# Kernel optimization log

Measured on AMD Instinct MI355X. Metric: run time of the kernel, lower is better.

## Reference

```python
import jax, jax.numpy as jnp
import numpy as np

B, N, E, H, L = 32, 128, 128, 8, 4      # graphs, nodes/graph, emb, heads, layers
ATOM, BOND, K, M = 64, 15, 32, 16384    # atom_dim, bond_dim, rbf_K, n_edges
CUTOFF = 5.0
DH = E // H


def _ln(x, g, b):
    mu = x.mean(-1, keepdims=True)
    var = ((x - mu) ** 2).mean(-1, keepdims=True)
    return (x - mu) / jnp.sqrt(var + 1e-5) * g + b


def setup_inputs() -> dict:
    key = jax.random.key(0)
    ks = iter(jax.random.split(key, 40))
    def rn(shape, s=1.0):
        return jax.random.normal(next(ks), shape, jnp.float32) * s
    inp = {}
    inp["x"] = rn((B * N, ATOM))
    inp["ei"] = jax.random.randint(next(ks), (2, M), 0, B * N, jnp.int32)
    bf = rn((M, BOND))
    dist = jax.random.uniform(next(ks), (M, 1), jnp.float32, 0.0, CUTOFF)
    inp["ea"] = jnp.concatenate([bf, dist], axis=1)  # last col = distance
    inp["pos"] = rn((B * N, 3), 2.0)
    inp["batch"] = jnp.repeat(jnp.arange(B, dtype=jnp.int32), N)  # contiguous equal-size graphs
    s = 0.02
    inp["Wproj"] = rn((ATOM, E), s); inp["bproj"] = jnp.zeros((E,), jnp.float32)
    EIN = BOND + K
    inp["Wlin"] = rn((EIN, E * E), s); inp["blin"] = jnp.zeros((E * E,), jnp.float32)
    inp["g_en"] = jnp.ones((E,), jnp.float32); inp["b_en"] = jnp.zeros((E,), jnp.float32)
    for nm in ["Wq", "Wk", "Wv", "Wo"]:
        inp[nm] = rn((L, E, E), s)
    for nm in ["bq", "bk", "bv", "bo"]:
        inp[nm] = jnp.zeros((L, E), jnp.float32)
    inp["g1"] = jnp.ones((L, E), jnp.float32); inp["b1"] = jnp.zeros((L, E), jnp.float32)
    inp["W1"] = rn((L, E, 2 * E), s); inp["bf1"] = jnp.zeros((L, 2 * E), jnp.float32)
    inp["W2"] = rn((L, 2 * E, E), s); inp["bf2"] = jnp.zeros((L, E), jnp.float32)
    inp["g2"] = jnp.ones((L, E), jnp.float32); inp["b2"] = jnp.zeros((L, E), jnp.float32)
    return inp


def reference(x, ei, ea, pos, batch, Wproj, bproj, Wlin, blin, g_en, b_en,
              Wq, bq, Wk, bk, Wv, bv, Wo, bo, g1, b1, W1, bf1, W2, bf2, g2, b2):
    # node projection
    h = x @ Wproj + bproj                              # [BN, E]
    # GaussianRBF on last edge-attr column
    d = jnp.clip(ea[:, -1], 0.0, 10.0)
    centers = jnp.linspace(0.0, CUTOFF, K)
    gamma = (CUTOFF / (K - 1)) ** -2
    rbf = jnp.exp(-gamma * (d[:, None] - centers) ** 2)  # [M, K]
    ea2 = jnp.concatenate([ea[:, :-1], rbf], axis=1)     # [M, BOND+K]
    # EdgeNetwork: gather -> per-edge matvec -> scatter-add -> LN
    m = (ea2 @ Wlin + blin).reshape(M, E, E)             # [M, E, E]
    msg = jnp.einsum('mef,mf->me', m, h[ei[1]])          # [M, E]
    agg = jnp.zeros_like(h).at[ei[0]].add(msg)
    h = _ln(h + agg, g_en, b_en)
    # batch-to-dense (equal-size contiguous graphs -> reshape)
    xp = h.reshape(B, N, E)
    pb = pos.reshape(B, N, 3)
    d2 = jnp.sum((pb[:, :, None, :] - pb[:, None, :, :]) ** 2, axis=-1)  # [B, N, N]
    db = jnp.where(d2 > 0, jnp.sqrt(jnp.where(d2 > 0, d2, 1.0)), 0.0)    # cdist
    mask = jnp.ones((B, N), bool)
    inv_sqrt_dh = 1.0 / np.sqrt(DH)
    for l in range(L):
        q = (xp @ Wq[l] + bq[l]).reshape(B, N, H, DH)
        k = (xp @ Wk[l] + bk[l]).reshape(B, N, H, DH)
        v = (xp @ Wv[l] + bv[l]).reshape(B, N, H, DH)
        sc = jnp.einsum('bihd,bjhd->bhij', q, k) * inv_sqrt_dh + db[:, None]
        sc = jnp.clip(sc, -10.0, 10.0)
        sc = jnp.where(mask[:, None, None, :], sc, -jnp.inf)
        a = jax.nn.softmax(sc, axis=-1)
        o = jnp.einsum('bhij,bjhd->bihd', a, v).reshape(B, N, E)
        att = o @ Wo[l] + bo[l]
        x1 = _ln(xp + att, g1[l], b1[l])
        ff = jax.nn.relu(x1 @ W1[l] + bf1[l]) @ W2[l] + bf2[l]
        xp = _ln(x1 + ff, g2[l], b2[l])
    mf = mask.astype(xp.dtype)[:, :, None]
    return (xp * mf).sum(1) / (mf.sum(1) + 1e-8)      # [B, E]
```

## Files before the change

kernel.cpp:

```cpp
#include <hip/hip_runtime.h>


typedef __attribute__((ext_vector_type(8))) short bf16x8;
typedef __attribute__((ext_vector_type(4))) float f32x4;
#define MFMA16(a, b, c) __builtin_amdgcn_mfma_f32_16x16x32_bf16(a, b, c, 0, 0, 0)

__device__ inline unsigned short f2bf(float f) {
  unsigned u = __float_as_uint(f);
  u = (u + 0x7FFF + ((u >> 16) & 1)) >> 16;
  return (unsigned short)u;
}
__device__ inline unsigned pack2(float a, float b) {
  return (unsigned)f2bf(a) | ((unsigned)f2bf(b) << 16);
}
__device__ inline float bf2f(unsigned short v) {
  return __uint_as_float(((unsigned)v) << 16);
}

__global__ __launch_bounds__(256) void k_setup(
    const float* __restrict__ x, const float* __restrict__ Wproj,
    const float* __restrict__ bproj, float* __restrict__ h,
    unsigned short* __restrict__ hb,
    const float* __restrict__ ea, float* __restrict__ ea2,
    const float* __restrict__ Wlin, const float* __restrict__ blin,
    unsigned short* __restrict__ wb,
    const float* __restrict__ Wq, const float* __restrict__ Wk,
    const float* __restrict__ Wv, const float* __restrict__ bq,
    const float* __restrict__ bk, const float* __restrict__ bv,
    unsigned short* __restrict__ qkvt, float* __restrict__ qkvb,
    const float* __restrict__ Wo, unsigned short* __restrict__ wot,
    const float* __restrict__ W1, unsigned short* __restrict__ w1t,
    const float* __restrict__ W2, unsigned short* __restrict__ w2t,
    float* __restrict__ agg) {
  __shared__ float xs[2][64];
  int blk = blockIdx.x, t = threadIdx.x;
  if (blk < 2048) {
    int sub = t >> 7, e = t & 127;
    int n = blk * 2 + sub;
    if (e < 64) xs[sub][e] = x[n * 64 + e];
    __syncthreads();
    float acc = bproj[e];
#pragma unroll
    for (int a = 0; a < 64; a++) acc += xs[sub][a] * Wproj[a * 128 + e];
    h[n * 128 + e] = acc;
    hb[n * 128 + e] = f2bf(acc);
    return;
  }
  int idx = (blk - 2048) * 256 + t;
  if (idx < 524288) {
    agg[idx] = 0.0f;
    return;
  }
  idx -= 524288;
  if (idx < 786432) {
    int m = idx / 48, c = idx % 48;
    float v;
    if (c < 15) {
      v = ea[m * 16 + c];
    } else if (c < 47) {
      int i = c - 15;
      float d = fminf(10.0f, fmaxf(0.0f, ea[m * 16 + 15]));
      float diff = d - 5.0f * (float)i / 31.0f;
      v = __expf(-38.44f * diff * diff);
    } else {
      v = 1.0f;
    }
    ea2[m * 48 + c] = v;
    return;
  }
  idx -= 786432;
  if (idx < 786432) {
    float v = (idx < 770048) ? Wlin[idx] : blin[idx - 770048];
    wb[idx] = f2bf(v);
    return;
  }
  idx -= 786432;
  if (idx < 196608) {
    int l = idx / 49152, r = idx % 49152;
    int j = r / 128, a = r % 128;
    int jj = j & 127;
    const float* W = (j < 128) ? Wq : (j < 256) ? Wk : Wv;
    qkvt[idx] = f2bf(W[l * 16384 + a * 128 + jj]);
    if (a == 0) {
      const float* bb = (j < 128) ? bq : (j < 256) ? bk : bv;
      qkvb[l * 384 + j] = bb[l * 128 + jj];
    }
    return;
  }
  idx -= 196608;
  if (idx < 65536) {
    int l = idx / 16384, r = idx % 16384;
    int a = r / 128, j = r % 128;
    wot[l * 16384 + j * 128 + a] = f2bf(Wo[idx]);
    return;
  }
  idx -= 65536;
  if (idx < 131072) {
    int l = idx / 32768, r = idx % 32768;
    int a = r / 256, j = r % 256;
    w1t[l * 32768 + j * 128 + a] = f2bf(W1[idx]);
    return;
  }
  idx -= 131072;
  {
    int l = idx / 32768, r = idx % 32768;
    int a = r / 128, j = r % 128;
    w2t[l * 32768 + j * 256 + a] = f2bf(W2[idx]);
  }
}

__global__ __launch_bounds__(256) void k_tbuild(const unsigned short* __restrict__ hb,
    const unsigned short* __restrict__ wb, unsigned short* __restrict__ T) {
  __shared__ unsigned short hs[16384];
  __shared__ unsigned short wsm[16384];
  int c = blockIdx.x >> 5;
  int n0 = (blockIdx.x & 31) << 7;
  int t = threadIdx.x;
  const uint4* hg = (const uint4*)hb + n0 * 16;
  const uint4* wg = (const uint4*)wb + c * 2048;
  uint4* hs4 = (uint4*)hs;
  uint4* ws4 = (uint4*)wsm;
#pragma unroll
  for (int i = 0; i < 8; i++) {
    int q = t + i * 256;
    int row = q >> 4, ch = q & 15;
    int d = row * 16 + (ch ^ (row & 7));
    hs4[d] = hg[q];
    ws4[d] = wg[q];
  }
  __syncthreads();
  int w = t >> 6, l = t & 63;
  int lr = l & 15, lg = l >> 4;
  f32x4 acc[2][8];
#pragma unroll
  for (int et = 0; et < 2; et++)
#pragma unroll
    for (int n = 0; n < 8; n++) acc[et][n] = (f32x4){0.f, 0.f, 0.f, 0.f};
#pragma unroll
  for (int s = 0; s < 4; s++) {
    bf16x8 af[2];
#pragma unroll
    for (int et = 0; et < 2; et++) {
      int er = w * 32 + et * 16 + lr;
      int ch = (s * 4 + lg) ^ (er & 7);
      af[et] = *(const bf16x8*)&wsm[(er * 16 + ch) * 8];
    }
#pragma unroll
    for (int n = 0; n < 8; n++) {
      int nr = n * 16 + lr;
      int ch = (s * 4 + lg) ^ (nr & 7);
      bf16x8 bfr = *(const bf16x8*)&hs[(nr * 16 + ch) * 8];
      acc[0][n] = MFMA16(af[0], bfr, acc[0][n]);
      acc[1][n] = MFMA16(af[1], bfr, acc[1][n]);
    }
  }
#pragma unroll
  for (int et = 0; et < 2; et++)
#pragma unroll
    for (int n = 0; n < 8; n++) {
      int node = n0 + n * 16 + lr;
      int e0 = w * 32 + et * 16 + lg * 4;
      uint2 pk;
      pk.x = pack2(acc[et][n][0], acc[et][n][1]);
      pk.y = pack2(acc[et][n][2], acc[et][n][3]);
      *(uint2*)&T[node * 6144 + c * 128 + e0] = pk;
    }
}

__global__ __launch_bounds__(128) void k_contract(const float* __restrict__ ea2,
    const int* __restrict__ ei, const unsigned short* __restrict__ T,
    float* __restrict__ agg) {
  int m = blockIdx.x, e = threadIdx.x;
  int src = ei[16384 + m], dst = ei[m];
  __shared__ float ec[48];
  if (e < 48) ec[e] = ea2[m * 48 + e];
  __syncthreads();
  const unsigned short* Ts = T + src * 6144;
  float acc = 0.0f;
#pragma unroll 6
  for (int c = 0; c < 48; c++) acc += ec[c] * bf2f(Ts[c * 128 + e]);
  atomicAdd(&agg[dst * 128 + e], acc);
}

__global__ __launch_bounds__(128) void k_ln(const float* __restrict__ in,
    const float* __restrict__ res, const float* __restrict__ g,
    const float* __restrict__ b, float* __restrict__ out) {
  int n = blockIdx.x, e = threadIdx.x;
  float v = in[n * 128 + e];
  if (res) v += res[n * 128 + e];
  float s = v, s2 = v * v;
#pragma unroll
  for (int o = 1; o < 64; o <<= 1) { s += __shfl_xor(s, o); s2 += __shfl_xor(s2, o); }
  __shared__ float r0[2], r1[2];
  int wid = e >> 6;
  if ((e & 63) == 0) { r0[wid] = s; r1[wid] = s2; }
  __syncthreads();
  float ts = r0[0] + r0[1], ts2 = r1[0] + r1[1];
  float mu = ts * (1.0f / 128.0f);
  float var = fmaxf(ts2 * (1.0f / 128.0f) - mu * mu, 0.0f);
  float inv = rsqrtf(var + 1e-5f);
  out[n * 128 + e] = (v - mu) * inv * g[e] + b[e];
}

__global__ __launch_bounds__(128) void k_dist(const float* __restrict__ pos, float* __restrict__ db) {
  int bi = blockIdx.x;
  int b = bi >> 7, i = bi & 127, j = threadIdx.x;
  float x0 = pos[(b * 128 + i) * 3 + 0];
  float y0 = pos[(b * 128 + i) * 3 + 1];
  float z0 = pos[(b * 128 + i) * 3 + 2];
  float dx = x0 - pos[(b * 128 + j) * 3 + 0];
  float dy = y0 - pos[(b * 128 + j) * 3 + 1];
  float dz = z0 - pos[(b * 128 + j) * 3 + 2];
  float d2 = dx * dx + dy * dy + dz * dz;
  db[b * 16384 + i * 128 + j] = (d2 > 0.0f) ? sqrtf(d2) : 0.0f;
}

template <int RELU, int RES, int LN, int KCH>
__global__ __launch_bounds__(256) void k_gemm(
    const float* __restrict__ A, const unsigned short* __restrict__ Bt,
    const float* __restrict__ bias, const float* __restrict__ res,
    const float* __restrict__ g, const float* __restrict__ bb,
    float* __restrict__ out, int ldc) {
  constexpr int K = KCH * 128;
  __shared__ unsigned short As[16384];
  __shared__ unsigned short Bs[16384];
  __shared__ float red[2][4][128];
  int t = threadIdx.x;
  int m0 = blockIdx.x << 7;
  int n0 = blockIdx.y << 7;
  uint4* As4 = (uint4*)As;
  uint4* Bs4 = (uint4*)Bs;
  int w = t >> 6, l = t & 63;
  int lr = l & 15, lg = l >> 4;

  f32x4 acc[2][8];
#pragma unroll
  for (int et = 0; et < 2; et++)
#pragma unroll
    for (int n = 0; n < 8; n++) acc[et][n] = (f32x4){0.f, 0.f, 0.f, 0.f};

  for (int kc = 0; kc < KCH; kc++) {
    if (kc) __syncthreads();
#pragma unroll
    for (int i = 0; i < 8; i++) {
      int q = t + i * 256;
      int row = q >> 4, ch = q & 15;
      int d = row * 16 + (ch ^ (row & 7));
      const float* ap = A + (size_t)(m0 + row) * K + kc * 128 + ch * 8;
      float4 fa = *(const float4*)ap;
      float4 fb = *(const float4*)(ap + 4);
      uint4 pk;
      pk.x = pack2(fa.x, fa.y); pk.y = pack2(fa.z, fa.w);
      pk.z = pack2(fb.x, fb.y); pk.w = pack2(fb.z, fb.w);
      As4[d] = pk;
      Bs4[d] = *((const uint4*)(Bt + (size_t)(n0 + row) * K + kc * 128) + ch);
    }
    __syncthreads();
#pragma unroll
    for (int s = 0; s < 4; s++) {
      bf16x8 af[2];
#pragma unroll
      for (int et = 0; et < 2; et++) {
        int er = w * 32 + et * 16 + lr;
        int ch = (s * 4 + lg) ^ (er & 7);
        af[et] = *(const bf16x8*)&Bs[(er * 16 + ch) * 8];
      }
#pragma unroll
      for (int n = 0; n < 8; n++) {
        int nr = n * 16 + lr;
        int ch = (s * 4 + lg) ^ (nr & 7);
        bf16x8 bfr = *(const bf16x8*)&As[(nr * 16 + ch) * 8];
        acc[0][n] = MFMA16(af[0], bfr, acc[0][n]);
        acc[1][n] = MFMA16(af[1], bfr, acc[1][n]);
      }
    }
  }

  float4 b4[2];
#pragma unroll
  for (int et = 0; et < 2; et++)
    b4[et] = *(const float4*)&bias[n0 + w * 32 + et * 16 + lg * 4];
  float v[2][8][4];
#pragma unroll
  for (int et = 0; et < 2; et++)
#pragma unroll
    for (int n = 0; n < 8; n++) {
      int node = m0 + n * 16 + lr;
      float4 rv;
      if (RES) rv = *(const float4*)&res[(size_t)node * 128 + w * 32 + et * 16 + lg * 4];
#pragma unroll
      for (int r = 0; r < 4; r++) {
        float xv = acc[et][n][r] + ((const float*)&b4[et])[r];
        if (RELU) xv = fmaxf(xv, 0.0f);
        if (RES) xv += ((const float*)&rv)[r];
        v[et][n][r] = xv;
      }
    }

  if (LN) {
    float s[8], s2[8];
#pragma unroll
    for (int n = 0; n < 8; n++) {
      float a = 0, b2s = 0;
#pragma unroll
      for (int et = 0; et < 2; et++)
#pragma unroll
        for (int r = 0; r < 4; r++) { a += v[et][n][r]; b2s += v[et][n][r] * v[et][n][r]; }
      s[n] = a; s2[n] = b2s;
    }
#pragma unroll
    for (int off = 16; off < 64; off <<= 1)
#pragma unroll
      for (int n = 0; n < 8; n++) { s[n] += __shfl_xor(s[n], off); s2[n] += __shfl_xor(s2[n], off); }
    if (l < 16) {
#pragma unroll
      for (int n = 0; n < 8; n++) { red[0][w][n * 16 + lr] = s[n]; red[1][w][n * 16 + lr] = s2[n]; }
    }
    __syncthreads();
    float4 g4[2], bb4[2];
#pragma unroll
    for (int et = 0; et < 2; et++) {
      g4[et]  = *(const float4*)&g[w * 32 + et * 16 + lg * 4];
      bb4[et] = *(const float4*)&bb[w * 32 + et * 16 + lg * 4];
    }
#pragma unroll
    for (int n = 0; n < 8; n++) {
      int nloc = n * 16 + lr;
      float ts  = red[0][0][nloc] + red[0][1][nloc] + red[0][2][nloc] + red[0][3][nloc];
      float ts2 = red[1][0][nloc] + red[1][1][nloc] + red[1][2][nloc] + red[1][3][nloc];
      float mu = ts * (1.0f / 128.0f);
      float var = fmaxf(ts2 * (1.0f / 128.0f) - mu * mu, 0.0f);
      float inv = rsqrtf(var + 1e-5f);
      int node = m0 + nloc;
#pragma unroll
      for (int et = 0; et < 2; et++) {
        float4 ov;
#pragma unroll
        for (int r = 0; r < 4; r++)
          ((float*)&ov)[r] = (v[et][n][r] - mu) * inv * ((const float*)&g4[et])[r] + ((const float*)&bb4[et])[r];
        *(float4*)&out[(size_t)node * ldc + w * 32 + et * 16 + lg * 4] = ov;
      }
    }
  } else {
#pragma unroll
    for (int et = 0; et < 2; et++)
#pragma unroll
      for (int n = 0; n < 8; n++) {
        int node = m0 + n * 16 + lr;
        float4 ov;
#pragma unroll
        for (int r = 0; r < 4; r++) ((float*)&ov)[r] = v[et][n][r];
        *(float4*)&out[(size_t)node * ldc + n0 + w * 32 + et * 16 + lg * 4] = ov;
      }
  }
}

__global__ __launch_bounds__(128) void k_attn(const float* __restrict__ qkv,
    const float* __restrict__ db, float* __restrict__ oatt) {
  __shared__ float ks[128][16], vs[128][16];
  int bh = blockIdx.x, b = bh >> 3, h = bh & 7;
  int i = threadIdx.x;
  int node = b * 128 + i;
  const float4* kr = (const float4*)(qkv + (size_t)node * 384 + 128 + h * 16);
  const float4* vr = (const float4*)(qkv + (size_t)node * 384 + 256 + h * 16);
#pragma unroll
  for (int d4 = 0; d4 < 4; d4++) {
    *(float4*)&ks[i][d4 * 4] = kr[d4];
    *(float4*)&vs[i][d4 * 4] = vr[d4];
  }
  float qr[16];
  const float4* qp = (const float4*)(qkv + (size_t)node * 384 + h * 16);
#pragma unroll
  for (int d4 = 0; d4 < 4; d4++) *(float4*)&qr[d4 * 4] = qp[d4];
  __syncthreads();
  const float4* dbr = (const float4*)(db + b * 16384 + i * 128);
  float rsum = 0.0f, o[16] = {};
  for (int j4 = 0; j4 < 32; j4++) {
    float4 dv = dbr[j4];
#pragma unroll
    for (int u = 0; u < 4; u++) {
      int j = j4 * 4 + u;
      float s = 0.0f;
#pragma unroll
      for (int d = 0; d < 16; d++) s += qr[d] * ks[j][d];
      s = s * 0.25f + ((const float*)&dv)[u];
      s = fminf(10.0f, fmaxf(-10.0f, s));
      float p = __expf(s);
      rsum += p;
#pragma unroll
      for (int d = 0; d < 16; d++) o[d] += p * vs[j][d];
    }
  }
  float r = 1.0f / rsum;
  float* op = oatt + (size_t)node * 128 + h * 16;
#pragma unroll
  for (int d4 = 0; d4 < 4; d4++)
    *(float4*)&op[d4 * 4] = make_float4(o[d4 * 4] * r, o[d4 * 4 + 1] * r, o[d4 * 4 + 2] * r, o[d4 * 4 + 3] * r);
}

__global__ __launch_bounds__(256) void k_layerout(
    const float* __restrict__ oatt, float* __restrict__ xp,
    const unsigned short* __restrict__ wot, const float* __restrict__ bo,
    const float* __restrict__ g1, const float* __restrict__ b1,
    const unsigned short* __restrict__ w1t, const float* __restrict__ bf1,
    const unsigned short* __restrict__ w2t, const float* __restrict__ bf2,
    const float* __restrict__ g2, const float* __restrict__ b2) {
  __shared__ unsigned short ffs[16384];
  __shared__ unsigned short x1s[8192];
  __shared__ unsigned short Bs[16384];
  __shared__ float red[2][4][64];
  int t = threadIdx.x;
  int m0 = blockIdx.x << 6;
  int w = t >> 6, l = t & 63, lr = l & 15, lg = l >> 4;

  {
    uint4* a4 = (uint4*)ffs;
#pragma unroll
    for (int i = 0; i < 4; i++) {
      int q = t + i * 256;
      int row = q >> 4, ch = q & 15;
      const float* ap = oatt + (size_t)(m0 + row) * 128 + ch * 8;
      float4 fa = *(const float4*)ap;
      float4 fb = *(const float4*)(ap + 4);
      uint4 pk;
      pk.x = pack2(fa.x, fa.y); pk.y = pack2(fa.z, fa.w);
      pk.z = pack2(fb.x, fb.y); pk.w = pack2(fb.z, fb.w);
      a4[row * 16 + (ch ^ (row & 7))] = pk;
    }
    uint4* b4p = (uint4*)Bs;
#pragma unroll
    for (int i = 0; i < 8; i++) {
      int q = t + i * 256;
      int row = q >> 4, ch = q & 15;
      b4p[row * 16 + (ch ^ (row & 7))] = *((const uint4*)(wot + (size_t)row * 128) + ch);
    }
  }
  __syncthreads();
  f32x4 acc[2][4];
#pragma unroll
  for (int et = 0; et < 2; et++)
#pragma unroll
    for (int n = 0; n < 4; n++) acc[et][n] = (f32x4){0.f, 0.f, 0.f, 0.f};
#pragma unroll
  for (int s = 0; s < 4; s++) {
    bf16x8 af[2];
#pragma unroll
    for (int et = 0; et < 2; et++) {
      int er = w * 32 + et * 16 + lr;
      int ch = (s * 4 + lg) ^ (er & 7);
      af[et] = *(const bf16x8*)&Bs[(er * 16 + ch) * 8];
    }
#pragma unroll
    for (int n = 0; n < 4; n++) {
      int nr = n * 16 + lr;
      int ch = (s * 4 + lg) ^ (nr & 7);
      bf16x8 bfr = *(const bf16x8*)&ffs[(nr * 16 + ch) * 8];
      acc[0][n] = MFMA16(af[0], bfr, acc[0][n]);
      acc[1][n] = MFMA16(af[1], bfr, acc[1][n]);
    }
  }
  float v1[2][4][4];
  {
    int e0 = w * 32 + lg * 4;
    float4 bo4[2] = { *(const float4*)&bo[e0], *(const float4*)&bo[e0 + 16] };
#pragma unroll
    for (int et = 0; et < 2; et++)
#pragma unroll
      for (int n = 0; n < 4; n++) {
        int node = m0 + n * 16 + lr;
        float4 rv = *(const float4*)&xp[(size_t)node * 128 + e0 + et * 16];
#pragma unroll
        for (int r = 0; r < 4; r++)
          v1[et][n][r] = acc[et][n][r] + ((const float*)&bo4[et])[r] + ((const float*)&rv)[r];
      }
    float s[4], s2[4];
#pragma unroll
    for (int n = 0; n < 4; n++) {
      float a = 0, b2s = 0;
#pragma unroll
      for (int et = 0; et < 2; et++)
#pragma unroll
        for (int r = 0; r < 4; r++) { a += v1[et][n][r]; b2s += v1[et][n][r] * v1[et][n][r]; }
      s[n] = a; s2[n] = b2s;
    }
#pragma unroll
    for (int off = 16; off < 64; off <<= 1)
#pragma unroll
      for (int n = 0; n < 4; n++) { s[n] += __shfl_xor(s[n], off); s2[n] += __shfl_xor(s2[n], off); }
    if (l < 16) {
#pragma unroll
      for (int n = 0; n < 4; n++) { red[0][w][n * 16 + lr] = s[n]; red[1][w][n * 16 + lr] = s2[n]; }
    }
    __syncthreads();
    float4 g4[2] = { *(const float4*)&g1[e0], *(const float4*)&g1[e0 + 16] };
    float4 bb4[2] = { *(const float4*)&b1[e0], *(const float4*)&b1[e0 + 16] };
#pragma unroll
    for (int n = 0; n < 4; n++) {
      int nloc = n * 16 + lr;
      float ts  = red[0][0][nloc] + red[0][1][nloc] + red[0][2][nloc] + red[0][3][nloc];
      float ts2 = red[1][0][nloc] + red[1][1][nloc] + red[1][2][nloc] + red[1][3][nloc];
      float mu = ts * (1.0f / 128.0f);
      float var = fmaxf(ts2 * (1.0f / 128.0f) - mu * mu, 0.0f);
      float inv = rsqrtf(var + 1e-5f);
#pragma unroll
      for (int et = 0; et < 2; et++) {
#pragma unroll
        for (int r = 0; r < 4; r++)
          v1[et][n][r] = (v1[et][n][r] - mu) * inv * ((const float*)&g4[et])[r] + ((const float*)&bb4[et])[r];
        int ch = w * 4 + et * 2 + (lg >> 1);
        uint2 pk;
        pk.x = pack2(v1[et][n][0], v1[et][n][1]);
        pk.y = pack2(v1[et][n][2], v1[et][n][3]);
        *(uint2*)&x1s[(nloc * 16 + (ch ^ (nloc & 7))) * 8 + (lg & 1) * 4] = pk;
      }
    }
  }
  __syncthreads();

  for (int ct = 0; ct < 2; ct++) {
    if (ct) __syncthreads();
    uint4* b4p = (uint4*)Bs;
#pragma unroll
    for (int i = 0; i < 8; i++) {
      int q = t + i * 256;
      int row = q >> 4, ch = q & 15;
      b4p[row * 16 + (ch ^ (row & 7))] =
          *((const uint4*)(w1t + (size_t)(ct * 128 + row) * 128) + ch);
    }
    __syncthreads();
#pragma unroll
    for (int et = 0; et < 2; et++)
#pragma unroll
      for (int n = 0; n < 4; n++) acc[et][n] = (f32x4){0.f, 0.f, 0.f, 0.f};
#pragma unroll
    for (int s = 0; s < 4; s++) {
      bf16x8 af[2];
#pragma unroll
      for (int et = 0; et < 2; et++) {
        int er = w * 32 + et * 16 + lr;
        int ch = (s * 4 + lg) ^ (er & 7);
        af[et] = *(const bf16x8*)&Bs[(er * 16 + ch) * 8];
      }
#pragma unroll
      for (int n = 0; n < 4; n++) {
        int nr = n * 16 + lr;
        int ch = (s * 4 + lg) ^ (nr & 7);
        bf16x8 bfr = *(const bf16x8*)&x1s[(nr * 16 + ch) * 8];
        acc[0][n] = MFMA16(af[0], bfr, acc[0][n]);
        acc[1][n] = MFMA16(af[1], bfr, acc[1][n]);
      }
    }
    int e0 = w * 32 + lg * 4;
    float4 bb0 = *(const float4*)&bf1[ct * 128 + e0];
    float4 bb1 = *(const float4*)&bf1[ct * 128 + e0 + 16];
#pragma unroll
    for (int et = 0; et < 2; et++) {
      const float* bbp = et ? (const float*)&bb1 : (const float*)&bb0;
#pragma unroll
      for (int n = 0; n < 4; n++) {
        int nloc = n * 16 + lr;
        float f0 = fmaxf(acc[et][n][0] + bbp[0], 0.0f);
        float f1 = fmaxf(acc[et][n][1] + bbp[1], 0.0f);
        float f2 = fmaxf(acc[et][n][2] + bbp[2], 0.0f);
        float f3 = fmaxf(acc[et][n][3] + bbp[3], 0.0f);
        int cg = ct * 16 + w * 4 + et * 2 + (lg >> 1);
        uint2 pk;
        pk.x = pack2(f0, f1);
        pk.y = pack2(f2, f3);
        *(uint2*)&ffs[(nloc * 32 + (cg ^ (nloc & 7))) * 8 + (lg & 1) * 4] = pk;
      }
    }
  }
  __syncthreads();

  f32x4 acc3[2][4];
#pragma unroll
  for (int et = 0; et < 2; et++)
#pragma unroll
    for (int n = 0; n < 4; n++) acc3[et][n] = (f32x4){0.f, 0.f, 0.f, 0.f};
  for (int kc = 0; kc < 2; kc++) {
    if (kc) __syncthreads();
    uint4* b4p = (uint4*)Bs;
#pragma unroll
    for (int i = 0; i < 8; i++) {
      int q = t + i * 256;
      int row = q >> 4, ch = q & 15;
      b4p[row * 16 + (ch ^ (row & 7))] =
          *((const uint4*)(w2t + (size_t)row * 256 + kc * 128) + ch);
    }
    __syncthreads();
#pragma unroll
    for (int s = 0; s < 4; s++) {
      bf16x8 af[2];
#pragma unroll
      for (int et = 0; et < 2; et++) {
        int er = w * 32 + et * 16 + lr;
        int ch = (s * 4 + lg) ^ (er & 7);
        af[et] = *(const bf16x8*)&Bs[(er * 16 + ch) * 8];
      }
#pragma unroll
      for (int n = 0; n < 4; n++) {
        int nr = n * 16 + lr;
        int gch = kc * 16 + s * 4 + lg;
        bf16x8 bfr = *(const bf16x8*)&ffs[(nr * 32 + (gch ^ (nr & 7))) * 8];
        acc3[0][n] = MFMA16(af[0], bfr, acc3[0][n]);
        acc3[1][n] = MFMA16(af[1], bfr, acc3[1][n]);
      }
    }
  }
  {
    int e0 = w * 32 + lg * 4;
    float4 bo4[2] = { *(const float4*)&bf2[e0], *(const float4*)&bf2[e0 + 16] };
    float v2[2][4][4];
#pragma unroll
    for (int et = 0; et < 2; et++)
#pragma unroll
      for (int n = 0; n < 4; n++)
#pragma unroll
        for (int r = 0; r < 4; r++)
          v2[et][n][r] = acc3[et][n][r] + ((const float*)&bo4[et])[r] + v1[et][n][r];
    float s[4], s2[4];
#pragma unroll
    for (int n = 0; n < 4; n++) {
      float a = 0, b2s = 0;
#pragma unroll
      for (int et = 0; et < 2; et++)
#pragma unroll
        for (int r = 0; r < 4; r++) { a += v2[et][n][r]; b2s += v2[et][n][r] * v2[et][n][r]; }
      s[n] = a; s2[n] = b2s;
    }
#pragma unroll
    for (int off = 16; off < 64; off <<= 1)
#pragma unroll
      for (int n = 0; n < 4; n++) { s[n] += __shfl_xor(s[n], off); s2[n] += __shfl_xor(s2[n], off); }
    __syncthreads();
    if (l < 16) {
#pragma unroll
      for (int n = 0; n < 4; n++) { red[0][w][n * 16 + lr] = s[n]; red[1][w][n * 16 + lr] = s2[n]; }
    }
    __syncthreads();
    float4 g4[2] = { *(const float4*)&g2[e0], *(const float4*)&g2[e0 + 16] };
    float4 bb4[2] = { *(const float4*)&b2[e0], *(const float4*)&b2[e0 + 16] };
#pragma unroll
    for (int n = 0; n < 4; n++) {
      int nloc = n * 16 + lr;
      float ts  = red[0][0][nloc] + red[0][1][nloc] + red[0][2][nloc] + red[0][3][nloc];
      float ts2 = red[1][0][nloc] + red[1][1][nloc] + red[1][2][nloc] + red[1][3][nloc];
      float mu = ts * (1.0f / 128.0f);
      float var = fmaxf(ts2 * (1.0f / 128.0f) - mu * mu, 0.0f);
      float inv = rsqrtf(var + 1e-5f);
      int node = m0 + nloc;
#pragma unroll
      for (int et = 0; et < 2; et++) {
        float4 ov;
#pragma unroll
        for (int r = 0; r < 4; r++)
          ((float*)&ov)[r] = (v2[et][n][r] - mu) * inv * ((const float*)&g4[et])[r] + ((const float*)&bb4[et])[r];
        *(float4*)&xp[(size_t)node * 128 + e0 + et * 16] = ov;
      }
    }
  }
}

__global__ __launch_bounds__(128) void k_pool(const float* __restrict__ xp, float* __restrict__ out) {
  int b = blockIdx.x, e = threadIdx.x;
  float s = 0.0f;
  for (int n = 0; n < 128; n++) s += xp[(b * 128 + n) * 128 + e];
  out[b * 128 + e] = s * (1.0f / 128.0f);
}

extern "C" void kernel_launch(void* const* d_in, const int* in_sizes, int n_in,
                              void* d_out, int out_size, void* d_ws, size_t ws_size,
                              hipStream_t stream) {
  const float* x     = (const float*)d_in[0];
  const int*   ei    = (const int*)  d_in[1];
  const float* ea    = (const float*)d_in[2];
  const float* pos   = (const float*)d_in[3];
  const float* Wproj = (const float*)d_in[5];
  const float* bproj = (const float*)d_in[6];
  const float* Wlin  = (const float*)d_in[7];
  const float* blin  = (const float*)d_in[8];
  const float* g_en  = (const float*)d_in[9];
  const float* b_en  = (const float*)d_in[10];
  const float* Wq    = (const float*)d_in[11];
  const float* Wk    = (const float*)d_in[12];
  const float* Wv    = (const float*)d_in[13];
  const float* Wo    = (const float*)d_in[14];
  const float* bq    = (const float*)d_in[15];
  const float* bk    = (const float*)d_in[16];
  const float* bv    = (const float*)d_in[17];
  const float* bo    = (const float*)d_in[18];
  const float* g1    = (const float*)d_in[19];
  const float* b1    = (const float*)d_in[20];
  const float* W1    = (const float*)d_in[21];
  const float* bf1   = (const float*)d_in[22];
  const float* W2    = (const float*)d_in[23];
  const float* bf2   = (const float*)d_in[24];
  const float* g2    = (const float*)d_in[25];
  const float* b2    = (const float*)d_in[26];

  float* ws = (float*)d_ws;
  float* ea2  = ws;
  float* hbuf = ea2  + 786432;
  float* agg  = hbuf + 524288;
  unsigned short* hbf  = (unsigned short*)(agg + 524288);
  unsigned short* wbf  = hbf + 524288;
  unsigned short* qkvt = wbf + 786432;
  unsigned short* wot  = qkvt + 196608;
  unsigned short* w1t  = wot + 65536;
  unsigned short* w2t  = w1t + 131072;
  float* qkvb = (float*)(w2t + 131072);
  float* base2 = qkvb + 1536;
  unsigned short* Tb = (unsigned short*)base2;
  float* db   = base2;
  float* xp   = db   + 524288;
  float* qkv  = xp   + 524288;
  float* oatt = qkv  + 1572864;

  k_setup<<<12288, 256, 0, stream>>>(x, Wproj, bproj, hbuf, hbf,
      ea, ea2, Wlin, blin, wbf, Wq, Wk, Wv, bq, bk, bv, qkvt, qkvb,
      Wo, wot, W1, w1t, W2, w2t, agg);
  k_tbuild<<<1536, 256, 0, stream>>>(hbf, wbf, Tb);
  k_contract<<<16384, 128, 0, stream>>>(ea2, ei, Tb, agg);
  k_ln<<<4096, 128, 0, stream>>>(agg, hbuf, g_en, b_en, xp);
  k_dist<<<4096, 128, 0, stream>>>(pos, db);

  for (int l = 0; l < 4; l++) {
    k_gemm<0, 0, 0, 1><<<dim3(32, 3), 256, 0, stream>>>(
        xp, qkvt + l * 49152, qkvb + l * 384, nullptr, nullptr, nullptr, qkv, 384);
    k_attn<<<256, 128, 0, stream>>>(qkv, db, oatt);
    k_layerout<<<64, 256, 0, stream>>>(oatt, xp,
        wot + l * 16384, bo + l * 128, g1 + l * 128, b1 + l * 128,
        w1t + l * 32768, bf1 + l * 256,
        w2t + l * 32768, bf2 + l * 128, g2 + l * 128, b2 + l * 128);
  }

  k_pool<<<32, 128, 0, stream>>>(xp, (float*)d_out);
}
```

Baseline: 336.8 us.

## Fuse edge message GEMM, LN+QKV, and next-layer QKV into layer-out kernel

Replaces the per-node T tensor build plus per-edge contraction with a single edge kernel. It gathers source-node features for 64 edges, runs an MFMA against each of the 48 weight slices, and accumulates the messages weighted by the edge attributes before doing atomic adds. The encoder LayerNorm is fused with the first QKV projection, each layer's output kernel also computes the next layer's QKV, and the distance matrix moves into the setup kernel. This removes the large T intermediate buffer and several launches. In exchange, each edge block reloads all 48 weight slices serially with a sync per slice, and only 256 blocks are launched.

```diff
diff --git a/kernel.cpp b/kernel.cpp
--- a/kernel.cpp
+++ b/kernel.cpp
@@ -12,9 +12,6 @@
 }
 __device__ inline unsigned pack2(float a, float b) {
   return (unsigned)f2bf(a) | ((unsigned)f2bf(b) << 16);
-}
-__device__ inline float bf2f(unsigned short v) {
-  return __uint_as_float(((unsigned)v) << 16);
 }
 
 __global__ __launch_bounds__(256) void k_setup(
@@ -31,7 +28,8 @@
     const float* __restrict__ Wo, unsigned short* __restrict__ wot,
     const float* __restrict__ W1, unsigned short* __restrict__ w1t,
     const float* __restrict__ W2, unsigned short* __restrict__ w2t,
-    float* __restrict__ agg) {
+    float* __restrict__ agg,
+    const float* __restrict__ pos, float* __restrict__ db) {
   __shared__ float xs[2][64];
   int blk = blockIdx.x, t = threadIdx.x;
   if (blk < 2048) {
@@ -47,10 +45,7 @@
     return;
   }
   int idx = (blk - 2048) * 256 + t;
-  if (idx < 524288) {
-    agg[idx] = 0.0f;
-    return;
-  }
+  if (idx < 524288) { agg[idx] = 0.0f; return; }
   idx -= 524288;
   if (idx < 786432) {
     int m = idx / 48, c = idx % 48;
@@ -102,171 +97,164 @@
     return;
   }
   idx -= 131072;
-  {
+  if (idx < 131072) {
     int l = idx / 32768, r = idx % 32768;
     int a = r / 128, j = r % 128;
     w2t[l * 32768 + j * 256 + a] = f2bf(W2[idx]);
-  }
-}
-
-__global__ __launch_bounds__(256) void k_tbuild(const unsigned short* __restrict__ hb,
-    const unsigned short* __restrict__ wb, unsigned short* __restrict__ T) {
-  __shared__ unsigned short hs[16384];
-  __shared__ unsigned short wsm[16384];
-  int c = blockIdx.x >> 5;
-  int n0 = (blockIdx.x & 31) << 7;
-  int t = threadIdx.x;
-  const uint4* hg = (const uint4*)hb + n0 * 16;
-  const uint4* wg = (const uint4*)wb + c * 2048;
+    return;
+  }
+  idx -= 131072;
+  {
+    int j = idx & 127, i2 = (idx >> 7) & 127, b = idx >> 14;
+    float x0 = pos[(b * 128 + i2) * 3 + 0];
+    float y0 = pos[(b * 128 + i2) * 3 + 1];
+    float z0 = pos[(b * 128 + i2) * 3 + 2];
+    float dx = x0 - pos[(b * 128 + j) * 3 + 0];
+    float dy = y0 - pos[(b * 128 + j) * 3 + 1];
+    float dz = z0 - pos[(b * 128 + j) * 3 + 2];
+    float d2 = dx * dx + dy * dy + dz * dz;
+    db[b * 16384 + i2 * 128 + j] = (d2 > 0.0f) ? sqrtf(d2) : 0.0f;
+  }
+}
+
+__global__ __launch_bounds__(256) void k_edge(const float* __restrict__ ea2,
+    const int* __restrict__ ei, const unsigned short* __restrict__ hbf,
+    const unsigned short* __restrict__ wb, float* __restrict__ agg) {
+  __shared__ unsigned short hs[8192];
+  __shared__ float et[64][48];
+  __shared__ unsigned short Bs[16384];
+  __shared__ int srcs[64], dsts[64];
+  int t = threadIdx.x, m0 = blockIdx.x * 64;
+  if (t < 64) { srcs[t] = ei[16384 + m0 + t]; dsts[t] = ei[m0 + t]; }
+  __syncthreads();
   uint4* hs4 = (uint4*)hs;
-  uint4* ws4 = (uint4*)wsm;
-#pragma unroll
-  for (int i = 0; i < 8; i++) {
+#pragma unroll
+  for (int i = 0; i < 4; i++) {
     int q = t + i * 256;
     int row = q >> 4, ch = q & 15;
-    int d = row * 16 + (ch ^ (row & 7));
-    hs4[d] = hg[q];
-    ws4[d] = wg[q];
-  }
-  __syncthreads();
-  int w = t >> 6, l = t & 63;
-  int lr = l & 15, lg = l >> 4;
-  f32x4 acc[2][8];
-#pragma unroll
-  for (int et = 0; et < 2; et++)
-#pragma unroll
-    for (int n = 0; n < 8; n++) acc[et][n] = (f32x4){0.f, 0.f, 0.f, 0.f};
-#pragma unroll
-  for (int s = 0; s < 4; s++) {
-    bf16x8 af[2];
-#pragma unroll
-    for (int et = 0; et < 2; et++) {
-      int er = w * 32 + et * 16 + lr;
-      int ch = (s * 4 + lg) ^ (er & 7);
-      af[et] = *(const bf16x8*)&wsm[(er * 16 + ch) * 8];
-    }
-#pragma unroll
-    for (int n = 0; n < 8; n++) {
-      int nr = n * 16 + lr;
-      int ch = (s * 4 + lg) ^ (nr & 7);
-      bf16x8 bfr = *(const bf16x8*)&hs[(nr * 16 + ch) * 8];
-      acc[0][n] = MFMA16(af[0], bfr, acc[0][n]);
-      acc[1][n] = MFMA16(af[1], bfr, acc[1][n]);
-    }
-  }
-#pragma unroll
-  for (int et = 0; et < 2; et++)
-#pragma unroll
-    for (int n = 0; n < 8; n++) {
-      int node = n0 + n * 16 + lr;
-      int e0 = w * 32 + et * 16 + lg * 4;
-      uint2 pk;
-      pk.x = pack2(acc[et][n][0], acc[et][n][1]);
-      pk.y = pack2(acc[et][n][2], acc[et][n][3]);
-      *(uint2*)&T[node * 6144 + c * 128 + e0] = pk;
-    }
-}
-
-__global__ __launch_bounds__(128) void k_contract(const float* __restrict__ ea2,
-    const int* __restrict__ ei, const unsigned short* __restrict__ T,
-    float* __restrict__ agg) {
-  int m = blockIdx.x, e = threadIdx.x;
-  int src = ei[16384 + m], dst = ei[m];
-  __shared__ float ec[48];
-  if (e < 48) ec[e] = ea2[m * 48 + e];
-  __syncthreads();
-  const unsigned short* Ts = T + src * 6144;
-  float acc = 0.0f;
-#pragma unroll 6
-  for (int c = 0; c < 48; c++) acc += ec[c] * bf2f(Ts[c * 128 + e]);
-  atomicAdd(&agg[dst * 128 + e], acc);
-}
-
-__global__ __launch_bounds__(128) void k_ln(const float* __restrict__ in,
-    const float* __restrict__ res, const float* __restrict__ g,
-    const float* __restrict__ b, float* __restrict__ out) {
-  int n = blockIdx.x, e = threadIdx.x;
-  float v = in[n * 128 + e];
-  if (res) v += res[n * 128 + e];
-  float s = v, s2 = v * v;
-#pragma unroll
-  for (int o = 1; o < 64; o <<= 1) { s += __shfl_xor(s, o); s2 += __shfl_xor(s2, o); }
-  __shared__ float r0[2], r1[2];
-  int wid = e >> 6;
-  if ((e & 63) == 0) { r0[wid] = s; r1[wid] = s2; }
-  __syncthreads();
-  float ts = r0[0] + r0[1], ts2 = r1[0] + r1[1];
-  float mu = ts * (1.0f / 128.0f);
-  float var = fmaxf(ts2 * (1.0f / 128.0f) - mu * mu, 0.0f);
-  float inv = rsqrtf(var + 1e-5f);
-  out[n * 128 + e] = (v - mu) * inv * g[e] + b[e];
-}
-
-__global__ __launch_bounds__(128) void k_dist(const float* __restrict__ pos, float* __restrict__ db) {
-  int bi = blockIdx.x;
-  int b = bi >> 7, i = bi & 127, j = threadIdx.x;
-  float x0 = pos[(b * 128 + i) * 3 + 0];
-  float y0 = pos[(b * 128 + i) * 3 + 1];
-  float z0 = pos[(b * 128 + i) * 3 + 2];
-  float dx = x0 - pos[(b * 128 + j) * 3 + 0];
-  float dy = y0 - pos[(b * 128 + j) * 3 + 1];
-  float dz = z0 - pos[(b * 128 + j) * 3 + 2];
-  float d2 = dx * dx + dy * dy + dz * dz;
-  db[b * 16384 + i * 128 + j] = (d2 > 0.0f) ? sqrtf(d2) : 0.0f;
-}
-
-template <int RELU, int RES, int LN, int KCH>
-__global__ __launch_bounds__(256) void k_gemm(
-    const float* __restrict__ A, const unsigned short* __restrict__ Bt,
-    const float* __restrict__ bias, const float* __restrict__ res,
-    const float* __restrict__ g, const float* __restrict__ bb,
-    float* __restrict__ out, int ldc) {
-  constexpr int K = KCH * 128;
-  __shared__ unsigned short As[16384];
-  __shared__ unsigned short Bs[16384];
-  __shared__ float red[2][4][128];
-  int t = threadIdx.x;
-  int m0 = blockIdx.x << 7;
-  int n0 = blockIdx.y << 7;
-  uint4* As4 = (uint4*)As;
+    hs4[row * 16 + (ch ^ (row & 7))] = ((const uint4*)(hbf + (size_t)srcs[row] * 128))[ch];
+  }
+#pragma unroll
+  for (int i = 0; i < 12; i++) {
+    int p = t + i * 256;
+    int mi = p / 48, c = p % 48;
+    et[mi][c] = ea2[(size_t)(m0 + mi) * 48 + c];
+  }
+  int w = t >> 6, l = t & 63, lr = l & 15, lg = l >> 4;
+  float msg[2][4][4] = {};
+  const f32x4 zf = {0.f, 0.f, 0.f, 0.f};
   uint4* Bs4 = (uint4*)Bs;
-  int w = t >> 6, l = t & 63;
-  int lr = l & 15, lg = l >> 4;
-
-  f32x4 acc[2][8];
-#pragma unroll
-  for (int et = 0; et < 2; et++)
-#pragma unroll
-    for (int n = 0; n < 8; n++) acc[et][n] = (f32x4){0.f, 0.f, 0.f, 0.f};
-
-  for (int kc = 0; kc < KCH; kc++) {
-    if (kc) __syncthreads();
+  for (int c = 0; c < 48; c++) {
+    __syncthreads();
 #pragma unroll
     for (int i = 0; i < 8; i++) {
       int q = t + i * 256;
       int row = q >> 4, ch = q & 15;
-      int d = row * 16 + (ch ^ (row & 7));
-      const float* ap = A + (size_t)(m0 + row) * K + kc * 128 + ch * 8;
-      float4 fa = *(const float4*)ap;
-      float4 fb = *(const float4*)(ap + 4);
-      uint4 pk;
-      pk.x = pack2(fa.x, fa.y); pk.y = pack2(fa.z, fa.w);
-      pk.z = pack2(fb.x, fb.y); pk.w = pack2(fb.z, fb.w);
-      As4[d] = pk;
-      Bs4[d] = *((const uint4*)(Bt + (size_t)(n0 + row) * K + kc * 128) + ch);
-    }
-    __syncthreads();
+      Bs4[row * 16 + (ch ^ (row & 7))] =
+          ((const uint4*)(wb + (size_t)c * 16384 + row * 128))[ch];
+    }
+    __syncthreads();
+    f32x4 pacc[2][4];
 #pragma unroll
     for (int s = 0; s < 4; s++) {
       bf16x8 af[2];
 #pragma unroll
-      for (int et = 0; et < 2; et++) {
-        int er = w * 32 + et * 16 + lr;
+      for (int e2 = 0; e2 < 2; e2++) {
+        int er = w * 32 + e2 * 16 + lr;
         int ch = (s * 4 + lg) ^ (er & 7);
-        af[et] = *(const bf16x8*)&Bs[(er * 16 + ch) * 8];
-      }
-#pragma unroll
-      for (int n = 0; n < 8; n++) {
+        af[e2] = *(const bf16x8*)&Bs[(er * 16 + ch) * 8];
+      }
+#pragma unroll
+      for (int n = 0; n < 4; n++) {
+        int nr = n * 16 + lr;
+        int ch = (s * 4 + lg) ^ (nr & 7);
+        bf16x8 bfr = *(const bf16x8*)&hs[(nr * 16 + ch) * 8];
+        if (s == 0) {
+          pacc[0][n] = MFMA16(af[0], bfr, zf);
+          pacc[1][n] = MFMA16(af[1], bfr, zf);
+        } else {
+          pacc[0][n] = MFMA16(af[0], bfr, pacc[0][n]);
+          pacc[1][n] = MFMA16(af[1], bfr, pacc[1][n]);
+        }
+      }
+    }
+#pragma unroll
+    for (int n = 0; n < 4; n++) {
+      float am = et[n * 16 + lr][c];
+#pragma unroll
+      for (int e2 = 0; e2 < 2; e2++)
+#pragma unroll
+        for (int r = 0; r < 4; r++)
+          msg[e2][n][r] += am * pacc[e2][n][r];
+    }
+  }
+#pragma unroll
+  for (int n = 0; n < 4; n++) {
+    int dst = dsts[n * 16 + lr];
+#pragma unroll
+    for (int e2 = 0; e2 < 2; e2++) {
+      int e0 = w * 32 + e2 * 16 + lg * 4;
+#pragma unroll
+      for (int r = 0; r < 4; r++)
+        atomicAdd(&agg[(size_t)dst * 128 + e0 + r], msg[e2][n][r]);
+    }
+  }
+}
+
+__global__ __launch_bounds__(256) void k_lnqkv(const float* __restrict__ agg,
+    const float* __restrict__ hbuf, const float* __restrict__ g_en,
+    const float* __restrict__ b_en, float* __restrict__ xp,
+    const unsigned short* __restrict__ qkvt, const float* __restrict__ qkvb,
+    float* __restrict__ qkv) {
+  __shared__ unsigned short As[8192];
+  __shared__ unsigned short Bs[16384];
+  int t = threadIdx.x, m0 = blockIdx.x * 64;
+  int w = t >> 6, l = t & 63, lr = l & 15, lg = l >> 4;
+  float ge0 = g_en[2 * l], ge1 = g_en[2 * l + 1];
+  float be0 = b_en[2 * l], be1 = b_en[2 * l + 1];
+  for (int i = 0; i < 16; i++) {
+    int r = i * 4 + w;
+    float2 av = ((const float2*)(agg + (size_t)(m0 + r) * 128))[l];
+    float2 hv = ((const float2*)(hbuf + (size_t)(m0 + r) * 128))[l];
+    float v0 = av.x + hv.x, v1 = av.y + hv.y;
+    float s = v0 + v1, s2 = v0 * v0 + v1 * v1;
+#pragma unroll
+    for (int o = 1; o < 64; o <<= 1) { s += __shfl_xor(s, o); s2 += __shfl_xor(s2, o); }
+    float mu = s * (1.0f / 128.0f);
+    float var = fmaxf(s2 * (1.0f / 128.0f) - mu * mu, 0.0f);
+    float inv = rsqrtf(var + 1e-5f);
+    float o0 = (v0 - mu) * inv * ge0 + be0;
+    float o1 = (v1 - mu) * inv * ge1 + be1;
+    ((float2*)(xp + (size_t)(m0 + r) * 128))[l] = make_float2(o0, o1);
+    ((unsigned*)As)[(r * 16 + ((l >> 2) ^ (r & 7))) * 4 + (l & 3)] = pack2(o0, o1);
+  }
+  uint4* Bs4 = (uint4*)Bs;
+  for (int cchunk = 0; cchunk < 3; cchunk++) {
+    __syncthreads();
+#pragma unroll
+    for (int i = 0; i < 8; i++) {
+      int q = t + i * 256;
+      int row = q >> 4, ch = q & 15;
+      Bs4[row * 16 + (ch ^ (row & 7))] =
+          ((const uint4*)(qkvt + (size_t)(cchunk * 128 + row) * 128))[ch];
+    }
+    __syncthreads();
+    f32x4 acc[2][4];
+#pragma unroll
+    for (int e2 = 0; e2 < 2; e2++)
+#pragma unroll
+      for (int n = 0; n < 4; n++) acc[e2][n] = (f32x4){0.f, 0.f, 0.f, 0.f};
+#pragma unroll
+    for (int s = 0; s < 4; s++) {
+      bf16x8 af[2];
+#pragma unroll
+      for (int e2 = 0; e2 < 2; e2++) {
+        int er = w * 32 + e2 * 16 + lr;
+        int ch = (s * 4 + lg) ^ (er & 7);
+        af[e2] = *(const bf16x8*)&Bs[(er * 16 + ch) * 8];
+      }
+#pragma unroll
+      for (int n = 0; n < 4; n++) {
         int nr = n * 16 + lr;
         int ch = (s * 4 + lg) ^ (nr & 7);
         bf16x8 bfr = *(const bf16x8*)&As[(nr * 16 + ch) * 8];
@@ -274,84 +262,19 @@
         acc[1][n] = MFMA16(af[1], bfr, acc[1][n]);
       }
     }
-  }
-
-  float4 b4[2];
-#pragma unroll
-  for (int et = 0; et < 2; et++)
-    b4[et] = *(const float4*)&bias[n0 + w * 32 + et * 16 + lg * 4];
-  float v[2][8][4];
-#pragma unroll
-  for (int et = 0; et < 2; et++)
-#pragma unroll
-    for (int n = 0; n < 8; n++) {
-      int node = m0 + n * 16 + lr;
-      float4 rv;
-      if (RES) rv = *(const float4*)&res[(size_t)node * 128 + w * 32 + et * 16 + lg * 4];
-#pragma unroll
-      for (int r = 0; r < 4; r++) {
-        float xv = acc[et][n][r] + ((const float*)&b4[et])[r];
-        if (RELU) xv = fmaxf(xv, 0.0f);
-        if (RES) xv += ((const float*)&rv)[r];
-        v[et][n][r] = xv;
-      }
-    }
-
-  if (LN) {
-    float s[8], s2[8];
-#pragma unroll
-    for (int n = 0; n < 8; n++) {
-      float a = 0, b2s = 0;
-#pragma unroll
-      for (int et = 0; et < 2; et++)
-#pragma unroll
-        for (int r = 0; r < 4; r++) { a += v[et][n][r]; b2s += v[et][n][r] * v[et][n][r]; }
-      s[n] = a; s2[n] = b2s;
-    }
-#pragma unroll
-    for (int off = 16; off < 64; off <<= 1)
-#pragma unroll
-      for (int n = 0; n < 8; n++) { s[n] += __shfl_xor(s[n], off); s2[n] += __shfl_xor(s2[n], off); }
-    if (l < 16) {
-#pragma unroll
-      for (int n = 0; n < 8; n++) { red[0][w][n * 16 + lr] = s[n]; red[1][w][n * 16 + lr] = s2[n]; }
-    }
-    __syncthreads();
-    float4 g4[2], bb4[2];
-#pragma unroll
-    for (int et = 0; et < 2; et++) {
-      g4[et]  = *(const float4*)&g[w * 32 + et * 16 + lg * 4];
-      bb4[et] = *(const float4*)&bb[w * 32 + et * 16 + lg * 4];
-    }
-#pragma unroll
-    for (int n = 0; n < 8; n++) {
-      int nloc = n * 16 + lr;
-      float ts  = red[0][0][nloc] + red[0][1][nloc] + red[0][2][nloc] + red[0][3][nloc];
-      float ts2 = red[1][0][nloc] + red[1][1][nloc] + red[1][2][nloc] + red[1][3][nloc];
-      float mu = ts * (1.0f / 128.0f);
-      float var = fmaxf(ts2 * (1.0f / 128.0f) - mu * mu, 0.0f);
-      float inv = rsqrtf(var + 1e-5f);
-      int node = m0 + nloc;
-#pragma unroll
-      for (int et = 0; et < 2; et++) {
-        float4 ov;
-#pragma unroll
-        for (int r = 0; r < 4; r++)
-          ((float*)&ov)[r] = (v[et][n][r] - mu) * inv * ((const float*)&g4[et])[r] + ((const float*)&bb4[et])[r];
-        *(float4*)&out[(size_t)node * ldc + w * 32 + et * 16 + lg * 4] = ov;
-      }
-    }
-  } else {
-#pragma unroll
-    for (int et = 0; et < 2; et++)
-#pragma unroll
-      for (int n = 0; n < 8; n++) {
+#pragma unroll
+    for (int e2 = 0; e2 < 2; e2++) {
+      int e0 = cchunk * 128 + w * 32 + e2 * 16 + lg * 4;
+      float4 bb = *(const float4*)&qkvb[e0];
+#pragma unroll
+      for (int n = 0; n < 4; n++) {
         int node = m0 + n * 16 + lr;
         float4 ov;
 #pragma unroll
-        for (int r = 0; r < 4; r++) ((float*)&ov)[r] = v[et][n][r];
-        *(float4*)&out[(size_t)node * ldc + n0 + w * 32 + et * 16 + lg * 4] = ov;
-      }
+        for (int r = 0; r < 4; r++) ((float*)&ov)[r] = acc[e2][n][r] + ((const float*)&bb)[r];
+        *(float4*)&qkv[(size_t)node * 384 + e0] = ov;
+      }
+    }
   }
 }
 
@@ -398,13 +321,16 @@
     *(float4*)&op[d4 * 4] = make_float4(o[d4 * 4] * r, o[d4 * 4 + 1] * r, o[d4 * 4 + 2] * r, o[d4 * 4 + 3] * r);
 }
 
-__global__ __launch_bounds__(256) void k_layerout(
+template <int QKV>
+__global__ __launch_bounds__(256) void k_loqkv(
     const float* __restrict__ oatt, float* __restrict__ xp,
     const unsigned short* __restrict__ wot, const float* __restrict__ bo,
     const float* __restrict__ g1, const float* __restrict__ b1,
     const unsigned short* __restrict__ w1t, const float* __restrict__ bf1,
     const unsigned short* __restrict__ w2t, const float* __restrict__ bf2,
-    const float* __restrict__ g2, const float* __restrict__ b2) {
+    const float* __restrict__ g2, const float* __restrict__ b2,
+    const unsigned short* __restrict__ qkvtn, const float* __restrict__ qkvbn,
+    float* __restrict__ qkv) {
   __shared__ unsigned short ffs[16384];
   __shared__ unsigned short x1s[8192];
   __shared__ unsigned short Bs[16384];
@@ -657,6 +583,64 @@
         for (int r = 0; r < 4; r++)
           ((float*)&ov)[r] = (v2[et][n][r] - mu) * inv * ((const float*)&g4[et])[r] + ((const float*)&bb4[et])[r];
         *(float4*)&xp[(size_t)node * 128 + e0 + et * 16] = ov;
+        if (QKV) {
+          int ch = w * 4 + et * 2 + (lg >> 1);
+          uint2 pk;
+          pk.x = pack2(((float*)&ov)[0], ((float*)&ov)[1]);
+          pk.y = pack2(((float*)&ov)[2], ((float*)&ov)[3]);
+          *(uint2*)&x1s[(nloc * 16 + (ch ^ (nloc & 7))) * 8 + (lg & 1) * 4] = pk;
+        }
+      }
+    }
+  }
+
+  if (QKV) {
+    uint4* Bs4 = (uint4*)Bs;
+    for (int cchunk = 0; cchunk < 3; cchunk++) {
+      __syncthreads();
+#pragma unroll
+      for (int i = 0; i < 8; i++) {
+        int q = t + i * 256;
+        int row = q >> 4, ch = q & 15;
+        Bs4[row * 16 + (ch ^ (row & 7))] =
+            ((const uint4*)(qkvtn + (size_t)(cchunk * 128 + row) * 128))[ch];
+      }
+      __syncthreads();
+      f32x4 qa[2][4];
+#pragma unroll
+      for (int e2 = 0; e2 < 2; e2++)
+#pragma unroll
+        for (int n = 0; n < 4; n++) qa[e2][n] = (f32x4){0.f, 0.f, 0.f, 0.f};
+#pragma unroll
+      for (int s = 0; s < 4; s++) {
+        bf16x8 af[2];
+#pragma unroll
+        for (int e2 = 0; e2 < 2; e2++) {
+          int er = w * 32 + e2 * 16 + lr;
+          int ch = (s * 4 + lg) ^ (er & 7);
+          af[e2] = *(const bf16x8*)&Bs[(er * 16 + ch) * 8];
+        }
+#pragma unroll
+        for (int n = 0; n < 4; n++) {
+          int nr = n * 16 + lr;
+          int ch = (s * 4 + lg) ^ (nr & 7);
+          bf16x8 bfr = *(const bf16x8*)&x1s[(nr * 16 + ch) * 8];
+          qa[0][n] = MFMA16(af[0], bfr, qa[0][n]);
+          qa[1][n] = MFMA16(af[1], bfr, qa[1][n]);
+        }
+      }
+#pragma unroll
+      for (int e2 = 0; e2 < 2; e2++) {
+        int e0 = cchunk * 128 + w * 32 + e2 * 16 + lg * 4;
+        float4 bb = *(const float4*)&qkvbn[e0];
+#pragma unroll
+        for (int n = 0; n < 4; n++) {
+          int node = m0 + n * 16 + lr;
+          float4 ov;
+#pragma unroll
+          for (int r = 0; r < 4; r++) ((float*)&ov)[r] = qa[e2][n][r] + ((const float*)&bb)[r];
+          *(float4*)&qkv[(size_t)node * 384 + e0] = ov;
+        }
       }
     }
   }
@@ -710,29 +694,32 @@
   unsigned short* w1t  = wot + 65536;
   unsigned short* w2t  = w1t + 131072;
   float* qkvb = (float*)(w2t + 131072);
-  float* base2 = qkvb + 1536;
-  unsigned short* Tb = (unsigned short*)base2;
-  float* db   = base2;
+  float* db   = qkvb + 1536;
   float* xp   = db   + 524288;
   float* qkv  = xp   + 524288;
   float* oatt = qkv  + 1572864;
 
-  k_setup<<<12288, 256, 0, stream>>>(x, Wproj, bproj, hbuf, hbf,
+  k_setup<<<14336, 256, 0, stream>>>(x, Wproj, bproj, hbuf, hbf,
       ea, ea2, Wlin, blin, wbf, Wq, Wk, Wv, bq, bk, bv, qkvt, qkvb,
-      Wo, wot, W1, w1t, W2, w2t, agg);
-  k_tbuild<<<1536, 256, 0, stream>>>(hbf, wbf, Tb);
-  k_contract<<<16384, 128, 0, stream>>>(ea2, ei, Tb, agg);
-  k_ln<<<4096, 128, 0, stream>>>(agg, hbuf, g_en, b_en, xp);
-  k_dist<<<4096, 128, 0, stream>>>(pos, db);
+      Wo, wot, W1, w1t, W2, w2t, agg, pos, db);
+  k_edge<<<256, 256, 0, stream>>>(ea2, ei, hbf, wbf, agg);
+  k_lnqkv<<<64, 256, 0, stream>>>(agg, hbuf, g_en, b_en, xp, qkvt, qkvb, qkv);
 
   for (int l = 0; l < 4; l++) {
-    k_gemm<0, 0, 0, 1><<<dim3(32, 3), 256, 0, stream>>>(
-        xp, qkvt + l * 49152, qkvb + l * 384, nullptr, nullptr, nullptr, qkv, 384);
     k_attn<<<256, 128, 0, stream>>>(qkv, db, oatt);
-    k_layerout<<<64, 256, 0, stream>>>(oatt, xp,
-        wot + l * 16384, bo + l * 128, g1 + l * 128, b1 + l * 128,
-        w1t + l * 32768, bf1 + l * 256,
-        w2t + l * 32768, bf2 + l * 128, g2 + l * 128, b2 + l * 128);
+    if (l < 3) {
+      k_loqkv<1><<<64, 256, 0, stream>>>(oatt, xp,
+          wot + l * 16384, bo + l * 128, g1 + l * 128, b1 + l * 128,
+          w1t + l * 32768, bf1 + l * 256,
+          w2t + l * 32768, bf2 + l * 128, g2 + l * 128, b2 + l * 128,
+          qkvt + (l + 1) * 49152, qkvb + (l + 1) * 384, qkv);
+    } else {
+      k_loqkv<0><<<64, 256, 0, stream>>>(oatt, xp,
+          wot + l * 16384, bo + l * 128, g1 + l * 128, b1 + l * 128,
+          w1t + l * 32768, bf1 + l * 256,
+          w2t + l * 32768, bf2 + l * 128, g2 + l * 128, b2 + l * 128,
+          nullptr, nullptr, nullptr);
+    }
   }
 
   k_pool<<<32, 128, 0, stream>>>(xp, (float*)d_out);
```

Measured after the change: 380.8 us. +13.1%, slower.
